# Kernel tuning notes

Measured on AMD Instinct MI355X. Metric: run time of the kernel, lower is better.

The kernel has to match this reference:

```python
import jax, jax.numpy as jnp
import numpy as np

B, S, IN_DIM, EMBED, HEADS, WINDOW = 2, 2048, 1024, 1024, 16, 256
HEAD_DIM = EMBED // HEADS
NEG_FILL = -9.0e15


def setup_inputs() -> dict:
    key = jax.random.key(0)
    k1, k2, k3, k4 = jax.random.split(key, 4)
    x = jax.random.normal(k1, (B, S, IN_DIM), dtype=jnp.float32)
    # padding_mask: positions with value 1 get zeroed in q/k/v (matches masked_fill semantics)
    padding_mask = jax.random.randint(k2, (B, S), 0, 2, dtype=jnp.int32)
    # xavier-uniform-like init scale for the linear weights
    lim_qkv = np.sqrt(6.0 / (IN_DIM + 3 * EMBED)).astype(np.float32)
    lim_o = np.sqrt(6.0 / (EMBED + EMBED)).astype(np.float32)
    Wqkv = jax.random.uniform(k3, (3 * EMBED, IN_DIM), jnp.float32, -lim_qkv, lim_qkv)
    bqkv = jnp.zeros((3 * EMBED,), jnp.float32)
    Wo = jax.random.uniform(k4, (EMBED, EMBED), jnp.float32, -lim_o, lim_o)
    bo = jnp.zeros((EMBED,), jnp.float32)
    return {"x": x, "padding_mask": padding_mask, "Wqkv": Wqkv, "bqkv": bqkv, "Wo": Wo, "bo": bo}


def reference(x, padding_mask, Wqkv, bqkv, Wo, bo):
    b, s, _ = x.shape
    h, hd, pad = HEADS, HEAD_DIM, WINDOW // 2
    # qkv projection: torch Linear is x @ W.T + b
    qkv = x @ Wqkv.T + bqkv                      # [B, S, 3E]
    qkv = qkv.reshape(b, s, h, 3 * hd).transpose(0, 2, 1, 3)  # [B, H, S, 3*hd]
    q, k, v = jnp.split(qkv, 3, axis=-1)          # each [B, H, S, hd]
    # zero out padded positions in q, k, v where padding_mask == 1
    pm = (padding_mask != 0)[:, None, :, None]    # [B, 1, S, 1]
    q = jnp.where(pm, 0.0, q)
    k = jnp.where(pm, 0.0, k)
    v = jnp.where(pm, 0.0, v)
    # dense banded scores: identical math to the unfold-based band compute
    scores = jnp.einsum("bhsd,bhtd->bhst", q, k)  # [B, H, S, S]
    idx = jnp.arange(s)
    band = jnp.abs(idx[None, :] - idx[:, None]) <= pad  # |i-j| <= window/2
    scores = jnp.where(band, scores, jnp.float32(NEG_FILL))
    scores = scores / jnp.sqrt(jnp.float32(hd))   # original scales AFTER the fill
    attn = jax.nn.softmax(scores, axis=-1)        # [B, H, S, S]
    vals = jnp.einsum("bhst,bhtd->bhsd", attn, v)  # [B, H, S, hd]
    vals = vals.transpose(0, 2, 1, 3).reshape(b, s, h * hd)  # [B, S, E]
    return vals @ Wo.T + bo
```

## Files before the change

kernel.cpp:

```cpp
#include <hip/hip_runtime.h>
#include <stdint.h>

#define S_LEN 2048
#define EMBED 1024
#define HEADS 16
#define HD 64
#define M_ROWS 4096
#define N_QKV 3072
#define KDIM 1024
#define SP 2336
#define CLP2 200

typedef __attribute__((ext_vector_type(8))) short short8;
typedef __attribute__((ext_vector_type(4))) float f32x4;

__device__ __forceinline__ unsigned short f2bf(float f) {
  union { float f; uint32_t u; } c; c.f = f;
  uint32_t u = c.u;
  u += 0x7fffu + ((u >> 16) & 1u);
  return (unsigned short)(u >> 16);
}

__device__ __forceinline__ void gload_lds16(const unsigned short* g, unsigned short* l) {
  __builtin_amdgcn_global_load_lds(
      (const __attribute__((address_space(1))) void*)g,
      (__attribute__((address_space(3))) void*)l, 16, 0, 0);
}

#define XQ 1048576
#define WQKVQ 786432
#define WOQ 262144
#define CVTQ (XQ + WQKVQ + WOQ)
__global__ __launch_bounds__(256) void cvt3_kernel(
    const float* __restrict__ x, const float* __restrict__ wqkv, const float* __restrict__ wo,
    unsigned short* __restrict__ xb, unsigned short* __restrict__ wqkvb, unsigned short* __restrict__ wob,
    unsigned short* __restrict__ vTp) {
  int i = blockIdx.x * blockDim.x + threadIdx.x;
  if (i < CVTQ) {
    const float* s; unsigned short* d; int off;
    if (i < XQ)               { s = x;    d = xb;    off = i; }
    else if (i < XQ + WQKVQ)  { s = wqkv; d = wqkvb; off = i - XQ; }
    else                      { s = wo;   d = wob;   off = i - XQ - WQKVQ; }
    float4 f = reinterpret_cast<const float4*>(s)[off];
    ushort4 o;
    o.x = f2bf(f.x); o.y = f2bf(f.y); o.z = f2bf(f.z); o.w = f2bf(f.w);
    reinterpret_cast<ushort4*>(d)[off] = o;
  } else {
    int j = i - CVTQ;
    int row = j / 72, p = j % 72;
    int off = row * 584 + (p < 32 ? p : 544 + (p - 32));
    reinterpret_cast<ushort4*>(vTp)[off] = (ushort4){0, 0, 0, 0};
  }
}

#define QKV_PHASE(DO_STAGE, NA, NB)                                            \
  {                                                                            \
    if (DO_STAGE) {                                                            \
      if (wave < 4) {                                                          \
        gload_lds16(g0 + k0, smem + sow + ldsu);                               \
        gload_lds16(g1 + k0, smem + sow + ldsu + 512);                         \
        gload_lds16(g2 + k0, smem + sow + ldsu + 1024);                        \
        gload_lds16(g3 + k0, smem + sow + ldsu + 1536);                        \
      } else {                                                                 \
        gload_lds16(g0 + k0, smem + sow + ldsu);                               \
        gload_lds16(g1 + k0, smem + sow + ldsu + 512);                         \
        gload_lds16(g2 + k0, smem + sow + ldsu + 1024);                        \
      }                                                                        \
    }                                                                          \
    __builtin_amdgcn_sched_barrier(0);                                         \
    if (wave < 4) asm volatile("s_waitcnt vmcnt(" #NA ")" ::: "memory");       \
    else          asm volatile("s_waitcnt vmcnt(" #NB ")" ::: "memory");       \
    __builtin_amdgcn_sched_barrier(0);                                         \
    __builtin_amdgcn_s_barrier();                                              \
    __builtin_amdgcn_sched_barrier(0);                                         \
    short8 af[4], bf[6];                                                       \
    _Pragma("unroll")                                                          \
    for (int mt = 0; mt < 4; mt++)                                             \
      af[mt] = *reinterpret_cast<const short8*>(&smem[so + abase + mt * 512]); \
    _Pragma("unroll")                                                          \
    for (int nt = 0; nt < 6; nt++)                                             \
      bf[nt] = *reinterpret_cast<const short8*>(&smem[so + bbase + nt * 512]); \
    asm volatile("s_waitcnt lgkmcnt(0)" ::: "memory");                         \
    __builtin_amdgcn_sched_barrier(0);                                         \
    __builtin_amdgcn_s_setprio(1);                                             \
    _Pragma("unroll")                                                          \
    for (int mt = 0; mt < 4; mt++)                                             \
      _Pragma("unroll")                                                        \
      for (int nt = 0; nt < 6; nt++)                                           \
        acc[mt][nt] = __builtin_amdgcn_mfma_f32_16x16x32_bf16(                 \
            af[mt], bf[nt], acc[mt][nt], 0, 0, 0);                             \
    __builtin_amdgcn_s_setprio(0);                                             \
    __builtin_amdgcn_sched_barrier(0);                                         \
  }

__global__ __launch_bounds__(512, 2) void gemm_qkv(
    const unsigned short* __restrict__ A, const unsigned short* __restrict__ Bm,
    const float* __restrict__ bias, const int* __restrict__ pm,
    unsigned short* __restrict__ qo, unsigned short* __restrict__ ko,
    unsigned short* __restrict__ vTp)
{
  __shared__ __align__(16) unsigned short smem[71680];
  const int t = threadIdx.x, wave = t >> 6, lane = t & 63;
  const int m16 = lane & 15, q4 = lane >> 4;
  const int wm = wave >> 1, wn = wave & 1;
  const int bid = blockIdx.x;
  const int mb = bid >> 4, nb = bid & 15;

  const int srow16 = lane >> 2;
  const int kseg = (lane & 3) ^ ((lane >> 3) & 3);
  const unsigned short *g0, *g1, *g2, *g3;
  int ldsu;
  if (wave < 4) {
    int u0 = wave * 4;
    g0 = A + (size_t)(mb * 256 + (u0 + 0) * 16 + srow16) * KDIM + kseg * 8;
    g1 = A + (size_t)(mb * 256 + (u0 + 1) * 16 + srow16) * KDIM + kseg * 8;
    g2 = A + (size_t)(mb * 256 + (u0 + 2) * 16 + srow16) * KDIM + kseg * 8;
    g3 = A + (size_t)(mb * 256 + (u0 + 3) * 16 + srow16) * KDIM + kseg * 8;
    ldsu = u0 * 512;
  } else {
    int u0 = (wave - 4) * 3;
    g0 = Bm + (size_t)(nb * 192 + (u0 + 0) * 16 + srow16) * KDIM + kseg * 8;
    g1 = Bm + (size_t)(nb * 192 + (u0 + 1) * 16 + srow16) * KDIM + kseg * 8;
    g2 = Bm + (size_t)(nb * 192 + (u0 + 2) * 16 + srow16) * KDIM + kseg * 8;
    g3 = g2;
    ldsu = 8192 + u0 * 512;
  }

  const int sa = q4 ^ ((m16 >> 1) & 3);
  const int abase = (wm * 64 + m16) * 32 + sa * 8;
  const int bbase = 8192 + (wn * 96 + m16) * 32 + sa * 8;

  f32x4 acc[4][6];
#pragma unroll
  for (int i_ = 0; i_ < 4; i_++)
#pragma unroll
    for (int j_ = 0; j_ < 6; j_++) acc[i_][j_] = (f32x4){0.f, 0.f, 0.f, 0.f};

  int so = 0, sow = 0, k0 = 0;
#pragma unroll
  for (int s = 0; s < 3; ++s) {
    if (wave < 4) {
      gload_lds16(g0 + k0, smem + sow + ldsu);
      gload_lds16(g1 + k0, smem + sow + ldsu + 512);
      gload_lds16(g2 + k0, smem + sow + ldsu + 1024);
      gload_lds16(g3 + k0, smem + sow + ldsu + 1536);
    } else {
      gload_lds16(g0 + k0, smem + sow + ldsu);
      gload_lds16(g1 + k0, smem + sow + ldsu + 512);
      gload_lds16(g2 + k0, smem + sow + ldsu + 1024);
    }
    sow += 14336; k0 += 32;
  }
  __builtin_amdgcn_sched_barrier(0);

  for (int h = 0; h < 29; ++h) {
    QKV_PHASE(true, 12, 9);
    so += 14336;  if (so  == 71680) so  = 0;
    sow += 14336; if (sow == 71680) sow = 0;
    k0 += 32;
  }
  QKV_PHASE(false, 8, 6);
  so += 14336; if (so == 71680) so = 0;
  QKV_PHASE(false, 4, 3);
  so += 14336; if (so == 71680) so = 0;
  QKV_PHASE(false, 0, 0);
  __syncthreads();

  float pmv[4][4];
#pragma unroll
  for (int mt = 0; mt < 4; mt++)
#pragma unroll
    for (int reg = 0; reg < 4; reg++) {
      int row = mb * 256 + wm * 64 + mt * 16 + q4 * 4 + reg;
      pmv[mt][reg] = (pm[row] != 0) ? 0.0f : 1.0f;
    }
#pragma unroll
  for (int nt = 0; nt < 6; nt++) {
    int cloc = wn * 96 + nt * 16 + m16;
    float bv = bias[nb * 192 + cloc];
#pragma unroll
    for (int mt = 0; mt < 4; mt++) {
#pragma unroll
      for (int reg = 0; reg < 4; reg++) {
        int rloc = wm * 64 + mt * 16 + q4 * 4 + reg;
        smem[rloc * CLP2 + cloc] = f2bf((acc[mt][nt][reg] + bv) * pmv[mt][reg]);
      }
    }
  }
  __syncthreads();
  const int s0 = mb * 256;
  const int bh = (s0 >> 11) * 16 + nb, s0l = s0 & 2047;
  {
    int r = t >> 1, half = t & 1;
    const unsigned short* sq = &smem[r * CLP2 + half * 32];
    unsigned short* dq = qo + ((size_t)(bh * 2048 + s0l + r)) * 64 + half * 32;
#pragma unroll
    for (int j = 0; j < 4; j++)
      *reinterpret_cast<short8*>(dq + j * 8) = *reinterpret_cast<const short8*>(sq + j * 8);
    const unsigned short* sk = &smem[r * CLP2 + 64 + half * 32];
    unsigned short* dk = ko + ((size_t)(bh * 2048 + s0l + r)) * 64 + half * 32;
#pragma unroll
    for (int j = 0; j < 4; j++)
      *reinterpret_cast<short8*>(dk + j * 8) = *reinterpret_cast<const short8*>(sk + j * 8);
  }
  {
    int d = t & 63, oct = t >> 6;
    unsigned short* dst = vTp + (size_t)(bh * 64 + d) * SP + 128 + s0l + oct * 32;
#pragma unroll
    for (int j8 = 0; j8 < 4; j8++) {
      short8 tmp;
#pragma unroll
      for (int jj = 0; jj < 8; jj++)
        tmp[jj] = (short)smem[(oct * 32 + j8 * 8 + jj) * CLP2 + 128 + d];
      *reinterpret_cast<short8*>(dst + j8 * 8) = tmp;
    }
  }
}

__global__ __launch_bounds__(256) void gemm_out(
    const unsigned short* __restrict__ A, const unsigned short* __restrict__ Bm,
    const float* __restrict__ bias, float* __restrict__ out)
{
  __shared__ __align__(16) unsigned char smemraw[49152];
  float* Cldf = (float*)smemraw;
  const int t = threadIdx.x, wave = t >> 6, lane = t & 63;
  const int m16 = lane & 15, q4 = lane >> 4;
  const int wm = wave >> 1, wn = wave & 1;
  const int flat = blockIdx.y * 8 + blockIdx.x;
  const int xcd = flat & 7, bi = flat >> 3;
  const int mb = xcd * 8 + (bi & 7);
  const int nb = bi >> 3;
  const int srow = lane >> 2, scol = (lane & 3) << 3;
  const unsigned short* pA  = A + (size_t)(mb * 64 + wave * 16 + srow) * KDIM + scol;
  const unsigned short* pB0 = Bm + (size_t)(nb * 128 + wave * 32 + srow) * KDIM + scol;
  const unsigned short* pB1 = pB0 + 16 * KDIM;
  f32x4 acc[2][4];
#pragma unroll
  for (int i_ = 0; i_ < 2; i_++)
#pragma unroll
    for (int j_ = 0; j_ < 4; j_++) acc[i_][j_] = (f32x4){0.f, 0.f, 0.f, 0.f};

  auto stage = [&](int buf, int kt) {
    unsigned short* As = (unsigned short*)smemraw + buf * 12288;
    unsigned short* Bs = As + 4096;
#pragma unroll
    for (int h = 0; h < 2; h++) {
      gload_lds16(pA + kt + h * 32,  As + h * 2048 + (wave * 16) * 32);
      gload_lds16(pB0 + kt + h * 32, Bs + h * 4096 + (wave * 32) * 32);
      gload_lds16(pB1 + kt + h * 32, Bs + h * 4096 + (wave * 32 + 16) * 32);
    }
  };

  stage(0, 0);
  __builtin_amdgcn_sched_barrier(0);
  int cur = 0;
  for (int kt = 0; kt < KDIM; kt += 64) {
    const bool st = (kt + 64 < KDIM);
    if (st) stage(cur ^ 1, kt + 64);
    __builtin_amdgcn_sched_barrier(0);
    if (st) asm volatile("s_waitcnt vmcnt(6)" ::: "memory");
    else    asm volatile("s_waitcnt vmcnt(0)" ::: "memory");
    __builtin_amdgcn_sched_barrier(0);
    __builtin_amdgcn_s_barrier();
    __builtin_amdgcn_sched_barrier(0);
    const unsigned short* As = (const unsigned short*)smemraw + cur * 12288;
    const unsigned short* Bs = As + 4096;
#pragma unroll
    for (int h = 0; h < 2; h++) {
      short8 af[2], bf[4];
#pragma unroll
      for (int mt = 0; mt < 2; mt++)
        af[mt] = *reinterpret_cast<const short8*>(&As[h * 2048 + (wm * 32 + mt * 16 + m16) * 32 + q4 * 8]);
#pragma unroll
      for (int nt = 0; nt < 4; nt++)
        bf[nt] = *reinterpret_cast<const short8*>(&Bs[h * 4096 + (wn * 64 + nt * 16 + m16) * 32 + q4 * 8]);
#pragma unroll
      for (int mt = 0; mt < 2; mt++)
#pragma unroll
        for (int nt = 0; nt < 4; nt++)
          acc[mt][nt] = __builtin_amdgcn_mfma_f32_16x16x32_bf16(af[mt], bf[nt], acc[mt][nt], 0, 0, 0);
    }
    __builtin_amdgcn_sched_barrier(0);
    __builtin_amdgcn_s_barrier();
    __builtin_amdgcn_sched_barrier(0);
    cur ^= 1;
  }

#pragma unroll
  for (int nt = 0; nt < 4; nt++) {
    int cloc = wn * 64 + nt * 16 + m16;
    float bv = bias[nb * 128 + cloc];
#pragma unroll
    for (int mt = 0; mt < 2; mt++) {
#pragma unroll
      for (int reg = 0; reg < 4; reg++) {
        int rloc = wm * 32 + mt * 16 + q4 * 4 + reg;
        Cldf[rloc * 132 + cloc] = acc[mt][nt][reg] + bv;
      }
    }
  }
  __syncthreads();
  {
    int r = t >> 2, seg = t & 3;
    float* dst = out + (size_t)(mb * 64 + r) * EMBED + nb * 128 + seg * 32;
    const float* srcl = &Cldf[r * 132 + seg * 32];
#pragma unroll
    for (int j = 0; j < 8; j++)
      *reinterpret_cast<float4*>(dst + j * 4) = *reinterpret_cast<const float4*>(srcl + j * 4);
  }
}

__global__ __launch_bounds__(256, 2) void attn_kernel(
    const unsigned short* __restrict__ q, const unsigned short* __restrict__ k,
    const unsigned short* __restrict__ vTp, unsigned short* __restrict__ vals)
{
  __shared__ __align__(16) unsigned short smem[40960];
  unsigned short* Ks = smem;
  unsigned short* Vs = smem + 20480;
  unsigned short* Pld = smem;

  const int bid = blockIdx.x;
  const int bh = bid & 31, qg = bid >> 5;
  const int lane = threadIdx.x & 63, wave = threadIdx.x >> 6;
  const int i0b = qg * 64;
  const int i0 = i0b + wave * 16;
  const int m16 = lane & 15, q4 = lane >> 4;

  const unsigned short* kbase = k + (size_t)bh * 2048 * 64;
#pragma unroll
  for (int n = 0; n < 10; n++) {
    int idx = (n * 4 + wave) * 64 + lane;
    int krow = idx >> 3, seg = idx & 7;
    int grow = i0b - 128 + krow;
    grow = grow < 0 ? 0 : (grow > 2047 ? 2047 : grow);
    int lseg = seg ^ (krow & 7);
    gload_lds16(kbase + (size_t)grow * 64 + lseg * 8, Ks + (n * 4 + wave) * 512);
  }
  const unsigned short* vbase = vTp + (size_t)bh * 64 * SP + i0b;
#pragma unroll
  for (int n = 0; n < 10; n++) {
    int idx = (n * 4 + wave) * 64 + lane;
    int vrow = idx / 40, rem = idx % 40;
    int l = (rem & ~7) | ((rem & 7) ^ (vrow & 7));
    gload_lds16(vbase + (size_t)vrow * SP + l * 8, Vs + (n * 4 + wave) * 512);
  }

  const unsigned short* qb = q + ((size_t)(bh * 2048 + i0 + m16)) * 64 + q4 * 8;
  short8 aq0 = *reinterpret_cast<const short8*>(qb);
  short8 aq1 = *reinterpret_cast<const short8*>(qb + 32);

  __syncthreads();

  float sum[4] = {0.f, 0.f, 0.f, 0.f};
  uint32_t pP[18][2];
#pragma unroll
  for (int ct = 0; ct < 18; ct++) {
    int r = (wave + ct) * 16 + m16;
    int js = i0b - 128 + r;
    const unsigned short* kr = Ks + r * 64;
    short8 b0 = *reinterpret_cast<const short8*>(kr + ((q4 ^ (r & 7)) * 8));
    short8 b1 = *reinterpret_cast<const short8*>(kr + (((q4 + 4) ^ (r & 7)) * 8));
    f32x4 a = {0.f, 0.f, 0.f, 0.f};
    a = __builtin_amdgcn_mfma_f32_16x16x32_bf16(aq0, b0, a, 0, 0, 0);
    a = __builtin_amdgcn_mfma_f32_16x16x32_bf16(aq1, b1, a, 0, 0, 0);
    unsigned short pe[4];
#pragma unroll
    for (int reg = 0; reg < 4; reg++) {
      int i = i0 + q4 * 4 + reg;
      bool valid = (js >= 0) && (js < 2048) && (js >= i - 128) && (js <= i + 128);
      float e = valid ? __expf(a[reg] * 0.125f) : 0.0f;
      sum[reg] += e;
      pe[reg] = f2bf(e);
    }
    pP[ct][0] = (uint32_t)pe[0] | ((uint32_t)pe[1] << 16);
    pP[ct][1] = (uint32_t)pe[2] | ((uint32_t)pe[3] << 16);
  }
  float rden[4];
#pragma unroll
  for (int reg = 0; reg < 4; reg++) {
    float s = sum[reg];
    s += __shfl_xor(s, 1);
    s += __shfl_xor(s, 2);
    s += __shfl_xor(s, 4);
    s += __shfl_xor(s, 8);
    rden[reg] = 1.0f / s;
  }

  __syncthreads();

  unsigned short* Pw = Pld + wave * 16 * 296;
#pragma unroll
  for (int ct = 0; ct < 18; ct++) {
    Pw[(q4 * 4 + 0) * 296 + ct * 16 + m16] = (unsigned short)(pP[ct][0] & 0xFFFF);
    Pw[(q4 * 4 + 1) * 296 + ct * 16 + m16] = (unsigned short)(pP[ct][0] >> 16);
    Pw[(q4 * 4 + 2) * 296 + ct * 16 + m16] = (unsigned short)(pP[ct][1] & 0xFFFF);
    Pw[(q4 * 4 + 3) * 296 + ct * 16 + m16] = (unsigned short)(pP[ct][1] >> 16);
  }
  short8 ap[9];
#pragma unroll
  for (int kc = 0; kc < 9; kc++)
    ap[kc] = *reinterpret_cast<const short8*>(&Pw[m16 * 296 + kc * 32 + q4 * 8]);

  const int b = bh >> 4, h = bh & 15;
#pragma unroll
  for (int dt = 0; dt < 4; dt++) {
    int vrow = dt * 16 + m16;
    const unsigned short* vr = Vs + vrow * 320;
    f32x4 av = {0.f, 0.f, 0.f, 0.f};
#pragma unroll
    for (int kc = 0; kc < 9; kc++) {
      int jseg = kc * 4 + wave * 2 + q4;
      if (jseg > 39) jseg = 39;
      int sseg = (jseg & ~7) | ((jseg & 7) ^ (vrow & 7));
      short8 bv = *reinterpret_cast<const short8*>(vr + sseg * 8);
      av = __builtin_amdgcn_mfma_f32_16x16x32_bf16(ap[kc], bv, av, 0, 0, 0);
    }
#pragma unroll
    for (int reg = 0; reg < 4; reg++)
      Pw[(q4 * 4 + reg) * 296 + dt * 16 + m16] = f2bf(av[reg] * rden[reg]);
  }
  {
    int srow = lane >> 2, seg = lane & 3;
    unsigned short* dst = vals + ((size_t)(b * 2048 + i0 + srow)) * 1024 + h * 64 + seg * 16;
    const unsigned short* srcl = &Pw[srow * 296 + seg * 16];
    *reinterpret_cast<short8*>(dst)     = *reinterpret_cast<const short8*>(srcl);
    *reinterpret_cast<short8*>(dst + 8) = *reinterpret_cast<const short8*>(srcl + 8);
  }
}

extern "C" void kernel_launch(void* const* d_in, const int* in_sizes, int n_in,
                              void* d_out, int out_size, void* d_ws, size_t ws_size,
                              hipStream_t stream) {
  const float* x    = (const float*)d_in[0];
  const int*   pm   = (const int*)d_in[1];
  const float* Wqkv = (const float*)d_in[2];
  const float* bqkv = (const float*)d_in[3];
  const float* Wo   = (const float*)d_in[4];
  const float* bo   = (const float*)d_in[5];
  float* out = (float*)d_out;
  char* ws = (char*)d_ws;

  unsigned short* xb    = (unsigned short*)(ws);
  unsigned short* vals  = (unsigned short*)(ws);
  unsigned short* Wqkvb = (unsigned short*)(ws +  8388608);
  unsigned short* Wob   = (unsigned short*)(ws + 14680064);
  unsigned short* qbuf  = (unsigned short*)(ws + 16777216);
  unsigned short* kbuf  = (unsigned short*)(ws + 25165824);
  unsigned short* vTp   = (unsigned short*)(ws + 33554432);

  cvt3_kernel<<<8768, 256, 0, stream>>>(x, Wqkv, Wo, xb, Wqkvb, Wob, vTp);
  gemm_qkv<<<256, 512, 0, stream>>>(xb, Wqkvb, bqkv, pm, qbuf, kbuf, vTp);
  attn_kernel<<<1024, 256, 0, stream>>>(qbuf, kbuf, vTp, vals);
  gemm_out<<<dim3(8, 64), 256, 0, stream>>>(vals, Wob, bo, out);
}
```

Baseline: 160.3 us.

## Read K and V directly from global memory in attention kernel, dropping LDS staging

The attention kernel no longer stages the K and V band tiles into shared memory with async global-to-LDS loads and block barriers. Each wave now reads its K rows and V^T segments straight from global memory (relying on cache reuse), and LDS holds only the per-wave P buffer. The smaller LDS footprint lets launch bounds go to 3 blocks per SM and removes two __syncthreads. The cost is redundant, latency-exposed global loads across overlapping waves and blocks in place of shared LDS reuse.

```diff
diff --git a/kernel.cpp b/kernel.cpp
--- a/kernel.cpp
+++ b/kernel.cpp
@@ -310,14 +310,11 @@
   }
 }
 
-__global__ __launch_bounds__(256, 2) void attn_kernel(
+__global__ __launch_bounds__(256, 3) void attn_kernel(
     const unsigned short* __restrict__ q, const unsigned short* __restrict__ k,
     const unsigned short* __restrict__ vTp, unsigned short* __restrict__ vals)
 {
-  __shared__ __align__(16) unsigned short smem[40960];
-  unsigned short* Ks = smem;
-  unsigned short* Vs = smem + 20480;
-  unsigned short* Pld = smem;
+  __shared__ __align__(16) unsigned short Pall[4 * 4736];
 
   const int bid = blockIdx.x;
   const int bh = bid & 31, qg = bid >> 5;
@@ -327,39 +324,20 @@
   const int m16 = lane & 15, q4 = lane >> 4;
 
   const unsigned short* kbase = k + (size_t)bh * 2048 * 64;
-#pragma unroll
-  for (int n = 0; n < 10; n++) {
-    int idx = (n * 4 + wave) * 64 + lane;
-    int krow = idx >> 3, seg = idx & 7;
-    int grow = i0b - 128 + krow;
-    grow = grow < 0 ? 0 : (grow > 2047 ? 2047 : grow);
-    int lseg = seg ^ (krow & 7);
-    gload_lds16(kbase + (size_t)grow * 64 + lseg * 8, Ks + (n * 4 + wave) * 512);
-  }
-  const unsigned short* vbase = vTp + (size_t)bh * 64 * SP + i0b;
-#pragma unroll
-  for (int n = 0; n < 10; n++) {
-    int idx = (n * 4 + wave) * 64 + lane;
-    int vrow = idx / 40, rem = idx % 40;
-    int l = (rem & ~7) | ((rem & 7) ^ (vrow & 7));
-    gload_lds16(vbase + (size_t)vrow * SP + l * 8, Vs + (n * 4 + wave) * 512);
-  }
-
   const unsigned short* qb = q + ((size_t)(bh * 2048 + i0 + m16)) * 64 + q4 * 8;
   short8 aq0 = *reinterpret_cast<const short8*>(qb);
   short8 aq1 = *reinterpret_cast<const short8*>(qb + 32);
 
-  __syncthreads();
-
   float sum[4] = {0.f, 0.f, 0.f, 0.f};
   uint32_t pP[18][2];
 #pragma unroll
   for (int ct = 0; ct < 18; ct++) {
     int r = (wave + ct) * 16 + m16;
     int js = i0b - 128 + r;
-    const unsigned short* kr = Ks + r * 64;
-    short8 b0 = *reinterpret_cast<const short8*>(kr + ((q4 ^ (r & 7)) * 8));
-    short8 b1 = *reinterpret_cast<const short8*>(kr + (((q4 + 4) ^ (r & 7)) * 8));
+    int grow = js < 0 ? 0 : (js > 2047 ? 2047 : js);
+    const unsigned short* kr = kbase + (size_t)grow * 64;
+    short8 b0 = *reinterpret_cast<const short8*>(kr + q4 * 8);
+    short8 b1 = *reinterpret_cast<const short8*>(kr + 32 + q4 * 8);
     f32x4 a = {0.f, 0.f, 0.f, 0.f};
     a = __builtin_amdgcn_mfma_f32_16x16x32_bf16(aq0, b0, a, 0, 0, 0);
     a = __builtin_amdgcn_mfma_f32_16x16x32_bf16(aq1, b1, a, 0, 0, 0);
@@ -386,9 +364,7 @@
     rden[reg] = 1.0f / s;
   }
 
-  __syncthreads();
-
-  unsigned short* Pw = Pld + wave * 16 * 296;
+  unsigned short* Pw = Pall + wave * 4736;
 #pragma unroll
   for (int ct = 0; ct < 18; ct++) {
     Pw[(q4 * 4 + 0) * 296 + ct * 16 + m16] = (unsigned short)(pP[ct][0] & 0xFFFF);
@@ -401,18 +377,18 @@
   for (int kc = 0; kc < 9; kc++)
     ap[kc] = *reinterpret_cast<const short8*>(&Pw[m16 * 296 + kc * 32 + q4 * 8]);
 
+  const unsigned short* vbase = vTp + (size_t)bh * 64 * SP + i0b;
   const int b = bh >> 4, h = bh & 15;
 #pragma unroll
   for (int dt = 0; dt < 4; dt++) {
     int vrow = dt * 16 + m16;
-    const unsigned short* vr = Vs + vrow * 320;
+    const unsigned short* vr = vbase + (size_t)vrow * SP;
     f32x4 av = {0.f, 0.f, 0.f, 0.f};
 #pragma unroll
     for (int kc = 0; kc < 9; kc++) {
       int jseg = kc * 4 + wave * 2 + q4;
       if (jseg > 39) jseg = 39;
-      int sseg = (jseg & ~7) | ((jseg & 7) ^ (vrow & 7));
-      short8 bv = *reinterpret_cast<const short8*>(vr + sseg * 8);
+      short8 bv = *reinterpret_cast<const short8*>(vr + jseg * 8);
       av = __builtin_amdgcn_mfma_f32_16x16x32_bf16(ap[kc], bv, av, 0, 0, 0);
     }
 #pragma unroll
```

Measured after the change: 168.7 us. 1.05x slower.
